# Performance work log

Hardware: AMD Instinct MI355X
Metric: run time of the kernel (lower is better)

The kernel has to match this reference:

```python
import jax, jax.numpy as jnp
import numpy as np

B = 64        # number of graphs in the batch
NPG = 1024    # nodes per graph (uniform batch_num_nodes)
N = B * NPG   # total nodes = 65536
D = 512       # input feature dim
DEG = 32      # average degree
K = 0.5       # keep-percent
DROP = NPG - int(np.ceil(K * NPG))  # number of lowest-score nodes zeroed per graph


def setup_inputs() -> dict:
    key = jax.random.key(0)
    k1, k2, k3, k4 = jax.random.split(key, 4)
    features = jax.random.normal(k1, (N, D), dtype=jnp.float32)
    # edges constrained inside each graph's node block (batched DGL graph is block-diagonal)
    offsets = (jnp.arange(B, dtype=jnp.int64) * NPG)[:, None]
    src = (jax.random.randint(k2, (B, NPG * DEG), 0, NPG, dtype=jnp.int64) + offsets).reshape(-1)
    dst = (jax.random.randint(k3, (B, NPG * DEG), 0, NPG, dtype=jnp.int64) + offsets).reshape(-1)
    # GraphConv(input_dim=D, out=1) parameters (glorot-ish scale)
    weight = jax.random.normal(k4, (D, 1), dtype=jnp.float32) * (1.0 / np.sqrt(D))
    bias = jnp.zeros((1,), dtype=jnp.float32)
    return {"features": features, "src": src, "dst": dst, "weight": weight, "bias": bias}


def reference(features, src, dst, weight, bias):
    # --- GraphConv(D -> 1, norm=True, bias=True, activation=relu) ---
    # old-DGL norm=True: symmetric normalization with in-degrees, norm=deg^-0.5 (0 for isolated)
    deg = jnp.zeros((N,), features.dtype).at[dst].add(1.0)
    norm = jnp.where(deg > 0, deg ** -0.5, 0.0)[:, None]          # [N,1]
    # in_feats > out_feats: project first, then aggregate scalars
    h = (features @ weight) * norm                                # [N,1]
    agg = jnp.zeros_like(h).at[dst].add(h[src])                   # sum over in-edges
    w = jax.nn.relu(agg * norm + bias)                            # [N,1] scores
    # --- per-graph top-k masking: zero the DROP smallest scores in each graph ---
    wb = w.reshape(B, NPG)
    ranks = jnp.argsort(jnp.argsort(wb, axis=1), axis=1)          # rank 0 = smallest
    wb = jnp.where(ranks < DROP, jnp.zeros((), wb.dtype), wb)
    # --- elementwise gating of features by (masked) scores ---
    return features * wb.reshape(N, 1)
```

## Files before the change

kernel.cpp:

```cpp
#include <hip/hip_runtime.h>

#define NTOT 65536
#define DIM  512
#define BGR  64
#define NPG  1024
#define DROPN 512
#define SLICES 8
#define DEG_BLOCKS (BGR * SLICES)
#define MV_BLOCKS 2048

typedef float vf4 __attribute__((ext_vector_type(4)));
typedef unsigned long long u64;

__global__ __launch_bounds__(256) void k1_matvec_deg(
        const float* __restrict__ X, const float* __restrict__ W,
        const int* __restrict__ dst,
        float* __restrict__ p, int* __restrict__ deg_part, int epg) {
    __shared__ int dl[NPG];
    if (blockIdx.x < DEG_BLOCKS) {
        const int b = blockIdx.x;
        const int g = b & (BGR - 1);
        const int slice = b >> 6;
        const int nbase = g * NPG;
        const int eps = epg / SLICES;
        for (int i = threadIdx.x; i < NPG; i += 256) dl[i] = 0;
        __syncthreads();
        const int4* d4 = (const int4*)(dst + (size_t)g * epg + (size_t)slice * eps);
        const int n4 = eps >> 2;
        for (int i = threadIdx.x; i < n4; i += 256) {
            int4 d = d4[i];
            atomicAdd(&dl[d.x - nbase], 1);
            atomicAdd(&dl[d.y - nbase], 1);
            atomicAdd(&dl[d.z - nbase], 1);
            atomicAdd(&dl[d.w - nbase], 1);
        }
        __syncthreads();
        int* op = deg_part + (size_t)slice * NTOT + nbase;
        for (int i = threadIdx.x; i < NPG; i += 256) op[i] = dl[i];
    } else {
        const int lane = threadIdx.x & 63;
        const int wid  = ((blockIdx.x - DEG_BLOCKS) * 256 + threadIdx.x) >> 6;
        const int nw   = (MV_BLOCKS * 256) >> 6;
        const vf4* wr = (const vf4*)W;
        const vf4 w0 = wr[lane], w1 = wr[lane + 64];
        for (int row = wid; row < NTOT; row += 2 * nw) {
            const int row2 = row + nw;
            const vf4* xr0 = (const vf4*)(X + (size_t)row  * DIM);
            const vf4* xr1 = (const vf4*)(X + (size_t)row2 * DIM);
            vf4 a0 = xr0[lane], a1 = xr0[lane + 64];
            vf4 b0 = xr1[lane], b1 = xr1[lane + 64];
            vf4 m0 = a0 * w0 + a1 * w1;
            vf4 m1 = b0 * w0 + b1 * w1;
            float s0 = m0[0] + m0[1] + m0[2] + m0[3];
            float s1 = m1[0] + m1[1] + m1[2] + m1[3];
            #pragma unroll
            for (int off = 32; off > 0; off >>= 1) {
                s0 += __shfl_down(s0, off, 64);
                s1 += __shfl_down(s1, off, 64);
            }
            if (lane == 0) { p[row] = s0; p[row2] = s1; }
        }
    }
}

__global__ __launch_bounds__(256) void k2_agg(
        const int* __restrict__ src, const int* __restrict__ dst,
        const float* __restrict__ p, const int* __restrict__ deg_part,
        float* __restrict__ agg_part, float* __restrict__ norm_out, int epg) {
    __shared__ float hl[NPG];
    __shared__ float al[NPG];
    const int b = blockIdx.x;
    const int g = b & (BGR - 1);
    const int slice = b >> 6;
    const int nbase = g * NPG;
    const int eps = epg / SLICES;
    for (int i = threadIdx.x; i < NPG; i += 256) {
        int d = 0;
        #pragma unroll
        for (int s = 0; s < SLICES; s++) d += deg_part[(size_t)s * NTOT + nbase + i];
        float nrm = d > 0 ? (1.0f / sqrtf((float)d)) : 0.f;
        hl[i] = p[nbase + i] * nrm;
        al[i] = 0.f;
        if (slice == 0) norm_out[nbase + i] = nrm;
    }
    __syncthreads();
    const int4* s4 = (const int4*)(src + (size_t)g * epg + (size_t)slice * eps);
    const int4* d4 = (const int4*)(dst + (size_t)g * epg + (size_t)slice * eps);
    const int n4 = eps >> 2;
    for (int i = threadIdx.x; i < n4; i += 256) {
        int4 s = s4[i];
        int4 d = d4[i];
        atomicAdd(&al[d.x - nbase], hl[s.x - nbase]);
        atomicAdd(&al[d.y - nbase], hl[s.y - nbase]);
        atomicAdd(&al[d.z - nbase], hl[s.z - nbase]);
        atomicAdd(&al[d.w - nbase], hl[s.w - nbase]);
    }
    __syncthreads();
    float* op = agg_part + (size_t)slice * NTOT + nbase;
    for (int i = threadIdx.x; i < NPG; i += 256) op[i] = al[i];
}

__global__ __launch_bounds__(1024) void k3_topk(
        const float* __restrict__ agg_part, const float* __restrict__ norm,
        const float* __restrict__ bias, float* __restrict__ gate) {
    __shared__ u64 sk[NPG];
    const int g = blockIdx.x;
    const int t = threadIdx.x;
    const int nbase = g * NPG;
    float a = 0.f;
    #pragma unroll
    for (int s = 0; s < SLICES; s++) a += agg_part[(size_t)s * NTOT + nbase + t];
    float w = a * norm[nbase + t] + bias[0];
    w = w > 0.f ? w : 0.f;
    u64 key = ((u64)__float_as_uint(w) << 32) | (unsigned int)t;
    for (int k = 2; k <= NPG; k <<= 1) {
        const bool up = ((t & k) == 0);
        for (int j = k >> 1; j >= 64; j >>= 1) {
            sk[t] = key;
            __syncthreads();
            u64 partner = sk[t ^ j];
            __syncthreads();
            bool takeMin = (((t & j) == 0) == up);
            key = takeMin ? (key < partner ? key : partner)
                          : (key > partner ? key : partner);
        }
        for (int j = ((k >> 1) < 32 ? (k >> 1) : 32); j >= 1; j >>= 1) {
            u64 partner = (u64)__shfl_xor((long long)key, j, 64);
            bool takeMin = (((t & j) == 0) == up);
            key = takeMin ? (key < partner ? key : partner)
                          : (key > partner ? key : partner);
        }
    }
    int idx = (int)(key & 0xffffffffull);
    float wv = __uint_as_float((unsigned int)(key >> 32));
    gate[nbase + idx] = (t < DROPN) ? 0.f : wv;
}

__global__ __launch_bounds__(256) void k4_gate(
        const float* __restrict__ X, const float* __restrict__ gate,
        float* __restrict__ out) {
    const int lane = threadIdx.x & 63;
    const int nw   = (gridDim.x * blockDim.x) >> 6;
    const int wid  = (blockIdx.x * blockDim.x + threadIdx.x) >> 6;
    for (int row = wid; row < NTOT; row += nw) {
        float g = gate[row];
        vf4* o = (vf4*)(out + (size_t)row * DIM);
        if (g == 0.f) {
            vf4 z = (vf4){0.f, 0.f, 0.f, 0.f};
            __builtin_nontemporal_store(z, &o[lane]);
            __builtin_nontemporal_store(z, &o[lane + 64]);
        } else {
            const vf4* xr = (const vf4*)(X + (size_t)row * DIM);
            vf4 a = xr[lane] * g;
            vf4 c = xr[lane + 64] * g;
            __builtin_nontemporal_store(a, &o[lane]);
            __builtin_nontemporal_store(c, &o[lane + 64]);
        }
    }
}

extern "C" void kernel_launch(void* const* d_in, const int* in_sizes, int n_in,
                              void* d_out, int out_size, void* d_ws, size_t ws_size,
                              hipStream_t stream) {
    const float* X    = (const float*)d_in[0];
    const int*   src  = (const int*)d_in[1];
    const int*   dst  = (const int*)d_in[2];
    const float* W    = (const float*)d_in[3];
    const float* bias = (const float*)d_in[4];
    float* out = (float*)d_out;
    int E   = in_sizes[1];
    int epg = E / BGR;

    float* ws       = (float*)d_ws;
    float* p        = ws;
    float* norm     = ws + 1 * NTOT;
    float* gate     = ws + 2 * NTOT;
    int*   deg_part = (int*)(ws + 3 * NTOT);
    float* agg_part = ws + (3 + SLICES) * NTOT;

    k1_matvec_deg<<<MV_BLOCKS + DEG_BLOCKS, 256, 0, stream>>>(X, W, dst, p, deg_part, epg);
    k2_agg<<<BGR * SLICES, 256, 0, stream>>>(src, dst, p, deg_part, agg_part, norm, epg);
    k3_topk<<<BGR, 1024, 0, stream>>>(agg_part, norm, bias, gate);
    k4_gate<<<2048, 256, 0, stream>>>(X, gate, out);
}
```

Measured before the change: 276.5 us.

## Fuse aggregation with top-k and drop slice partials for degree and aggregation

Degree counting now uses one block per graph and writes the normalization directly, with no partial-degree buffers. The edge aggregation is merged into the top-k kernel, one 1024-thread block per graph, so the aggregated scores stay in shared memory. This removes one launch and the partial-sum buffers and their global round trips. In exchange, the degree and aggregation passes run on only 64 blocks, so each block walks all 32K edges of its graph with less parallelism per edge.

```diff
diff --git a/kernel.cpp b/kernel.cpp
--- a/kernel.cpp
+++ b/kernel.cpp
@@ -5,8 +5,7 @@
 #define BGR  64
 #define NPG  1024
 #define DROPN 512
-#define SLICES 8
-#define DEG_BLOCKS (BGR * SLICES)
+#define DEG_BLOCKS 64
 #define MV_BLOCKS 2048
 
 typedef float vf4 __attribute__((ext_vector_type(4)));
@@ -15,18 +14,15 @@
 __global__ __launch_bounds__(256) void k1_matvec_deg(
         const float* __restrict__ X, const float* __restrict__ W,
         const int* __restrict__ dst,
-        float* __restrict__ p, int* __restrict__ deg_part, int epg) {
+        float* __restrict__ p, float* __restrict__ norm, int epg) {
     __shared__ int dl[NPG];
     if (blockIdx.x < DEG_BLOCKS) {
-        const int b = blockIdx.x;
-        const int g = b & (BGR - 1);
-        const int slice = b >> 6;
+        const int g = blockIdx.x;
         const int nbase = g * NPG;
-        const int eps = epg / SLICES;
         for (int i = threadIdx.x; i < NPG; i += 256) dl[i] = 0;
         __syncthreads();
-        const int4* d4 = (const int4*)(dst + (size_t)g * epg + (size_t)slice * eps);
-        const int n4 = eps >> 2;
+        const int4* d4 = (const int4*)(dst + (size_t)g * epg);
+        const int n4 = epg >> 2;
         for (int i = threadIdx.x; i < n4; i += 256) {
             int4 d = d4[i];
             atomicAdd(&dl[d.x - nbase], 1);
@@ -35,8 +31,10 @@
             atomicAdd(&dl[d.w - nbase], 1);
         }
         __syncthreads();
-        int* op = deg_part + (size_t)slice * NTOT + nbase;
-        for (int i = threadIdx.x; i < NPG; i += 256) op[i] = dl[i];
+        for (int i = threadIdx.x; i < NPG; i += 256) {
+            int d = dl[i];
+            norm[nbase + i] = d > 0 ? rsqrtf((float)d) : 0.f;
+        }
     } else {
         const int lane = threadIdx.x & 63;
         const int wid  = ((blockIdx.x - DEG_BLOCKS) * 256 + threadIdx.x) >> 6;
@@ -63,31 +61,24 @@
     }
 }
 
-__global__ __launch_bounds__(256) void k2_agg(
+__global__ __launch_bounds__(1024) void k2_agg_topk(
         const int* __restrict__ src, const int* __restrict__ dst,
-        const float* __restrict__ p, const int* __restrict__ deg_part,
-        float* __restrict__ agg_part, float* __restrict__ norm_out, int epg) {
+        const float* __restrict__ p, const float* __restrict__ norm,
+        const float* __restrict__ bias, float* __restrict__ gate, int epg) {
     __shared__ float hl[NPG];
     __shared__ float al[NPG];
-    const int b = blockIdx.x;
-    const int g = b & (BGR - 1);
-    const int slice = b >> 6;
+    __shared__ u64 sk[NPG];
+    const int g = blockIdx.x;
+    const int t = threadIdx.x;
     const int nbase = g * NPG;
-    const int eps = epg / SLICES;
-    for (int i = threadIdx.x; i < NPG; i += 256) {
-        int d = 0;
-        #pragma unroll
-        for (int s = 0; s < SLICES; s++) d += deg_part[(size_t)s * NTOT + nbase + i];
-        float nrm = d > 0 ? (1.0f / sqrtf((float)d)) : 0.f;
-        hl[i] = p[nbase + i] * nrm;
-        al[i] = 0.f;
-        if (slice == 0) norm_out[nbase + i] = nrm;
-    }
+    const float nrm = norm[nbase + t];
+    hl[t] = p[nbase + t] * nrm;
+    al[t] = 0.f;
     __syncthreads();
-    const int4* s4 = (const int4*)(src + (size_t)g * epg + (size_t)slice * eps);
-    const int4* d4 = (const int4*)(dst + (size_t)g * epg + (size_t)slice * eps);
-    const int n4 = eps >> 2;
-    for (int i = threadIdx.x; i < n4; i += 256) {
+    const int4* s4 = (const int4*)(src + (size_t)g * epg);
+    const int4* d4 = (const int4*)(dst + (size_t)g * epg);
+    const int n4 = epg >> 2;
+    for (int i = t; i < n4; i += 1024) {
         int4 s = s4[i];
         int4 d = d4[i];
         atomicAdd(&al[d.x - nbase], hl[s.x - nbase]);
@@ -96,21 +87,7 @@
         atomicAdd(&al[d.w - nbase], hl[s.w - nbase]);
     }
     __syncthreads();
-    float* op = agg_part + (size_t)slice * NTOT + nbase;
-    for (int i = threadIdx.x; i < NPG; i += 256) op[i] = al[i];
-}
-
-__global__ __launch_bounds__(1024) void k3_topk(
-        const float* __restrict__ agg_part, const float* __restrict__ norm,
-        const float* __restrict__ bias, float* __restrict__ gate) {
-    __shared__ u64 sk[NPG];
-    const int g = blockIdx.x;
-    const int t = threadIdx.x;
-    const int nbase = g * NPG;
-    float a = 0.f;
-    #pragma unroll
-    for (int s = 0; s < SLICES; s++) a += agg_part[(size_t)s * NTOT + nbase + t];
-    float w = a * norm[nbase + t] + bias[0];
+    float w = al[t] * nrm + bias[0];
     w = w > 0.f ? w : 0.f;
     u64 key = ((u64)__float_as_uint(w) << 32) | (unsigned int)t;
     for (int k = 2; k <= NPG; k <<= 1) {
@@ -136,7 +113,7 @@
     gate[nbase + idx] = (t < DROPN) ? 0.f : wv;
 }
 
-__global__ __launch_bounds__(256) void k4_gate(
+__global__ __launch_bounds__(256) void k3_gate(
         const float* __restrict__ X, const float* __restrict__ gate,
         float* __restrict__ out) {
     const int lane = threadIdx.x & 63;
@@ -171,15 +148,12 @@
     int E   = in_sizes[1];
     int epg = E / BGR;
 
-    float* ws       = (float*)d_ws;
-    float* p        = ws;
-    float* norm     = ws + 1 * NTOT;
-    float* gate     = ws + 2 * NTOT;
-    int*   deg_part = (int*)(ws + 3 * NTOT);
-    float* agg_part = ws + (3 + SLICES) * NTOT;
+    float* ws   = (float*)d_ws;
+    float* p    = ws;
+    float* norm = ws + 1 * NTOT;
+    float* gate = ws + 2 * NTOT;
 
-    k1_matvec_deg<<<MV_BLOCKS + DEG_BLOCKS, 256, 0, stream>>>(X, W, dst, p, deg_part, epg);
-    k2_agg<<<BGR * SLICES, 256, 0, stream>>>(src, dst, p, deg_part, agg_part, norm, epg);
-    k3_topk<<<BGR, 1024, 0, stream>>>(agg_part, norm, bias, gate);
-    k4_gate<<<2048, 256, 0, stream>>>(X, gate, out);
+    k1_matvec_deg<<<DEG_BLOCKS + MV_BLOCKS, 256, 0, stream>>>(X, W, dst, p, norm, epg);
+    k2_agg_topk<<<BGR, 1024, 0, stream>>>(src, dst, p, norm, bias, gate, epg);
+    k3_gate<<<2048, 256, 0, stream>>>(X, gate, out);
 }
```

Result: slower. 307.6 us (+11.2%).

## Replace bitonic top-k sort with radix select and fold degree normalization into k1

Applied to the files above, without the earlier changes.

The per-graph full bitonic sort of 1024 keys in k3 is replaced with a four-pass byte-wise radix select. It finds the threshold value and breaks ties by thread index to match stable argsort ordering, avoiding the many shared-memory barrier stages of the sort. Degree counting now uses one block per graph over all edges and writes the rsqrt norm directly. This removes the slice partials and the reduction over them in k2, but concentrates more serial atomic work in fewer blocks during the matvec phase.

```diff
diff --git a/kernel.cpp b/kernel.cpp
--- a/kernel.cpp
+++ b/kernel.cpp
@@ -6,7 +6,7 @@
 #define NPG  1024
 #define DROPN 512
 #define SLICES 8
-#define DEG_BLOCKS (BGR * SLICES)
+#define DEG_BLOCKS 64
 #define MV_BLOCKS 2048
 
 typedef float vf4 __attribute__((ext_vector_type(4)));
@@ -15,18 +15,15 @@
 __global__ __launch_bounds__(256) void k1_matvec_deg(
         const float* __restrict__ X, const float* __restrict__ W,
         const int* __restrict__ dst,
-        float* __restrict__ p, int* __restrict__ deg_part, int epg) {
+        float* __restrict__ p, float* __restrict__ norm, int epg) {
     __shared__ int dl[NPG];
     if (blockIdx.x < DEG_BLOCKS) {
-        const int b = blockIdx.x;
-        const int g = b & (BGR - 1);
-        const int slice = b >> 6;
+        const int g = blockIdx.x;
         const int nbase = g * NPG;
-        const int eps = epg / SLICES;
         for (int i = threadIdx.x; i < NPG; i += 256) dl[i] = 0;
         __syncthreads();
-        const int4* d4 = (const int4*)(dst + (size_t)g * epg + (size_t)slice * eps);
-        const int n4 = eps >> 2;
+        const int4* d4 = (const int4*)(dst + (size_t)g * epg);
+        const int n4 = epg >> 2;
         for (int i = threadIdx.x; i < n4; i += 256) {
             int4 d = d4[i];
             atomicAdd(&dl[d.x - nbase], 1);
@@ -35,8 +32,10 @@
             atomicAdd(&dl[d.w - nbase], 1);
         }
         __syncthreads();
-        int* op = deg_part + (size_t)slice * NTOT + nbase;
-        for (int i = threadIdx.x; i < NPG; i += 256) op[i] = dl[i];
+        for (int i = threadIdx.x; i < NPG; i += 256) {
+            int d = dl[i];
+            norm[nbase + i] = d > 0 ? rsqrtf((float)d) : 0.f;
+        }
     } else {
         const int lane = threadIdx.x & 63;
         const int wid  = ((blockIdx.x - DEG_BLOCKS) * 256 + threadIdx.x) >> 6;
@@ -65,8 +64,8 @@
 
 __global__ __launch_bounds__(256) void k2_agg(
         const int* __restrict__ src, const int* __restrict__ dst,
-        const float* __restrict__ p, const int* __restrict__ deg_part,
-        float* __restrict__ agg_part, float* __restrict__ norm_out, int epg) {
+        const float* __restrict__ p, const float* __restrict__ norm,
+        float* __restrict__ agg_part, int epg) {
     __shared__ float hl[NPG];
     __shared__ float al[NPG];
     const int b = blockIdx.x;
@@ -75,13 +74,8 @@
     const int nbase = g * NPG;
     const int eps = epg / SLICES;
     for (int i = threadIdx.x; i < NPG; i += 256) {
-        int d = 0;
-        #pragma unroll
-        for (int s = 0; s < SLICES; s++) d += deg_part[(size_t)s * NTOT + nbase + i];
-        float nrm = d > 0 ? (1.0f / sqrtf((float)d)) : 0.f;
-        hl[i] = p[nbase + i] * nrm;
+        hl[i] = p[nbase + i] * norm[nbase + i];
         al[i] = 0.f;
-        if (slice == 0) norm_out[nbase + i] = nrm;
     }
     __syncthreads();
     const int4* s4 = (const int4*)(src + (size_t)g * epg + (size_t)slice * eps);
@@ -103,37 +97,65 @@
 __global__ __launch_bounds__(1024) void k3_topk(
         const float* __restrict__ agg_part, const float* __restrict__ norm,
         const float* __restrict__ bias, float* __restrict__ gate) {
-    __shared__ u64 sk[NPG];
+    __shared__ unsigned int hist[256];
+    __shared__ unsigned int selbin, selkp;
+    __shared__ unsigned int wsum[16];
     const int g = blockIdx.x;
     const int t = threadIdx.x;
+    const int lane = t & 63;
+    const int wid  = t >> 6;
     const int nbase = g * NPG;
     float a = 0.f;
     #pragma unroll
     for (int s = 0; s < SLICES; s++) a += agg_part[(size_t)s * NTOT + nbase + t];
     float w = a * norm[nbase + t] + bias[0];
     w = w > 0.f ? w : 0.f;
-    u64 key = ((u64)__float_as_uint(w) << 32) | (unsigned int)t;
-    for (int k = 2; k <= NPG; k <<= 1) {
-        const bool up = ((t & k) == 0);
-        for (int j = k >> 1; j >= 64; j >>= 1) {
-            sk[t] = key;
-            __syncthreads();
-            u64 partner = sk[t ^ j];
-            __syncthreads();
-            bool takeMin = (((t & j) == 0) == up);
-            key = takeMin ? (key < partner ? key : partner)
-                          : (key > partner ? key : partner);
-        }
-        for (int j = ((k >> 1) < 32 ? (k >> 1) : 32); j >= 1; j >>= 1) {
-            u64 partner = (u64)__shfl_xor((long long)key, j, 64);
-            bool takeMin = (((t & j) == 0) == up);
-            key = takeMin ? (key < partner ? key : partner)
-                          : (key > partner ? key : partner);
-        }
-    }
-    int idx = (int)(key & 0xffffffffull);
-    float wv = __uint_as_float((unsigned int)(key >> 32));
-    gate[nbase + idx] = (t < DROPN) ? 0.f : wv;
+    const unsigned int v = __float_as_uint(w);
+    bool act = true;
+    unsigned int kp = DROPN;
+    unsigned int T = 0;
+    #pragma unroll
+    for (int shift = 24; shift >= 0; shift -= 8) {
+        if (t < 256) hist[t] = 0;
+        __syncthreads();
+        const unsigned int byte = (v >> shift) & 255u;
+        if (act) atomicAdd(&hist[byte], 1u);
+        __syncthreads();
+        if (t < 64) {
+            unsigned int h0 = hist[t*4], h1 = hist[t*4+1], h2 = hist[t*4+2], h3 = hist[t*4+3];
+            unsigned int lsum = h0 + h1 + h2 + h3;
+            unsigned int x = lsum;
+            #pragma unroll
+            for (int off = 1; off < 64; off <<= 1) {
+                unsigned int y = (unsigned int)__shfl_up((int)x, off, 64);
+                if (lane >= off) x += y;
+            }
+            unsigned int excl = x - lsum;
+            hist[t*4]   = excl + h0;
+            hist[t*4+1] = excl + h0 + h1;
+            hist[t*4+2] = excl + h0 + h1 + h2;
+            hist[t*4+3] = excl + h0 + h1 + h2 + h3;
+        }
+        __syncthreads();
+        if (t < 256) {
+            unsigned int lo = (t == 0) ? 0u : hist[t-1];
+            unsigned int hi = hist[t];
+            if (lo <= kp && kp < hi) { selbin = (unsigned int)t; selkp = kp - lo; }
+        }
+        __syncthreads();
+        const unsigned int b = selbin;
+        kp = selkp;
+        act = act && (byte == b);
+        T |= b << shift;
+    }
+    u64 bal = __ballot(act);
+    if (lane == 0) wsum[wid] = (unsigned int)__popcll(bal);
+    __syncthreads();
+    unsigned int wpre = 0;
+    for (int i = 0; i < wid; i++) wpre += wsum[i];
+    unsigned int eqrank = wpre + (unsigned int)__popcll(bal & ((1ull << lane) - 1ull));
+    bool keep = act ? (eqrank >= kp) : (v > T);
+    gate[nbase + t] = keep ? w : 0.f;
 }
 
 __global__ __launch_bounds__(256) void k4_gate(
@@ -175,11 +197,10 @@
     float* p        = ws;
     float* norm     = ws + 1 * NTOT;
     float* gate     = ws + 2 * NTOT;
-    int*   deg_part = (int*)(ws + 3 * NTOT);
-    float* agg_part = ws + (3 + SLICES) * NTOT;
-
-    k1_matvec_deg<<<MV_BLOCKS + DEG_BLOCKS, 256, 0, stream>>>(X, W, dst, p, deg_part, epg);
-    k2_agg<<<BGR * SLICES, 256, 0, stream>>>(src, dst, p, deg_part, agg_part, norm, epg);
+    float* agg_part = ws + 3 * NTOT;
+
+    k1_matvec_deg<<<DEG_BLOCKS + MV_BLOCKS, 256, 0, stream>>>(X, W, dst, p, norm, epg);
+    k2_agg<<<BGR * SLICES, 256, 0, stream>>>(src, dst, p, norm, agg_part, epg);
     k3_topk<<<BGR, 1024, 0, stream>>>(agg_part, norm, bias, gate);
     k4_gate<<<2048, 256, 0, stream>>>(X, gate, out);
 }
```

Measured after the change: 276.9 us. About the same (+0.2%).
